# Performance work log

Measured on AMD Instinct MI355X. Metric: run time of the kernel, lower is better.

The kernel has to match this reference:

```python
import jax, jax.numpy as jnp
import numpy as np

EPS = 1e-5  # torch BatchNorm2d default eps
K = 16


def _bn_relu(x, gamma, beta):
    # training-mode BatchNorm over (B, N, k) per channel (last axis), biased variance
    mean = x.mean(axis=(0, 1, 2), keepdims=True)
    var = x.var(axis=(0, 1, 2), keepdims=True)
    xn = (x - mean) * jax.lax.rsqrt(var + EPS)
    return jax.nn.relu(xn * gamma + beta)


def _knn_idx(xyz, k):
    # squared pairwise distances (monotone in cdist p=2, same topk ordering)
    sq = jnp.sum(xyz * xyz, axis=-1)                       # (B, N)
    d2 = sq[:, :, None] + sq[:, None, :] - 2.0 * jnp.einsum('bnd,bmd->bnm', xyz, xyz)
    return jax.lax.top_k(-d2, k)[1]                        # (B, N, k) smallest dists


def setup_inputs() -> dict:
    key = jax.random.key(0)
    ks = jax.random.split(key, 4)
    B, N, C, O = 4, 4096, 64, 128
    return {
        'feats': jax.random.normal(ks[0], (B, N, C), jnp.float32),
        'xyz': jax.random.normal(ks[1], (B, N, 3), jnp.float32),
        'w1': jax.random.normal(ks[2], (O, 2 * C), jnp.float32) * 0.05,
        'gamma1': jnp.ones((O,), jnp.float32),
        'beta1': jnp.zeros((O,), jnp.float32),
        'w2': jax.random.normal(ks[3], (O, O), jnp.float32) * 0.05,
        'gamma2': jnp.ones((O,), jnp.float32),
        'beta2': jnp.zeros((O,), jnp.float32),
    }


def reference(feats, xyz, w1, gamma1, beta1, w2, gamma2, beta2):
    B, N, C = feats.shape
    k = min(K, N)
    idx = _knn_idx(xyz, k)                                  # (B, N, k)
    neighbor = jax.vmap(lambda f, i: f[i])(feats, idx)      # (B, N, k, C) gather
    center = feats[:, :, None, :]                           # (B, N, 1, C)
    edge = jnp.concatenate(
        [jnp.broadcast_to(center, neighbor.shape), neighbor - center], axis=-1
    )                                                       # (B, N, k, 2C)
    h = jnp.einsum('bnkc,oc->bnko', edge, w1)               # 1x1 conv #1
    h = _bn_relu(h, gamma1, beta1)
    h = jnp.einsum('bnkc,oc->bnko', h, w2)                  # 1x1 conv #2
    h = _bn_relu(h, gamma2, beta2)
    return h.max(axis=2)                                    # max over neighbors -> (B, N, O)
```

## Files before the change

### kernel.cpp

```cpp
#include <hip/hip_runtime.h>
#include <hip/hip_bf16.h>
#include <stdint.h>


#define B_ 4
#define N_ 4096
#define C_ 64
#define O_ 128
#define K_ 16
#define NQ_ (B_*N_)
#define ROWS_ (NQ_*K_)
#define EPS_ 1e-5f
#define M1_ 10
#define M2_ 20

typedef float f32x4 __attribute__((ext_vector_type(4)));
typedef short s16x8 __attribute__((ext_vector_type(8)));

__device__ __forceinline__ unsigned short f2bf(float f) {
  union { float f; uint32_t u; } x; x.f = f;
  uint32_t r = x.u + 0x7FFFu + ((x.u >> 16) & 1u);
  return (unsigned short)(r >> 16);
}
__device__ __forceinline__ uint32_t pack2(float a, float b) {
  return (uint32_t)f2bf(a) | ((uint32_t)f2bf(b) << 16);
}
__device__ __forceinline__ float bfl(uint32_t x) { return __uint_as_float(x << 16); }
__device__ __forceinline__ float bfh(uint32_t x) { return __uint_as_float(x & 0xFFFF0000u); }

template<bool SELF>
__device__ __forceinline__ void knn_scan(const float4* pts, int j0, int jq,
                                         float nx, float ny, float nz, float qw,
                                         float* lst) {
#pragma unroll 4
  for (int j = j0; j < j0 + N_/16; ++j) {
    float4 P = pts[j];
    float d2 = fmaf(P.z, nz, fmaf(P.y, ny, fmaf(P.x, nx, P.w + qw)));
    uint32_t kb = (__float_as_uint(d2) & 0xFFFFF000u) | (uint32_t)j;
    float k = __uint_as_float(kb);
    if (SELF) k = (j == jq) ? 1e30f : k;
#pragma unroll
    for (int s = M1_-1; s >= 1; --s)
      lst[s] = __builtin_amdgcn_fmed3f(lst[s-1], lst[s], k);
    lst[0] = fminf(lst[0], k);
  }
}

__global__ __launch_bounds__(1024) void knn_kernel(const float* __restrict__ xyz,
                                                   int* __restrict__ idx_out) {
  __shared__ float4 pts[N_];
  __shared__ float mbuf[8 * 64 * (M2_+1)];
  const int t = threadIdx.x;
  const int lane = t & 63;
  const int w = t >> 6;
  const int qbase = blockIdx.x * 64;
  const float* xb = xyz + (size_t)(qbase >> 12) * N_ * 3;
  for (int i = t; i < N_; i += 1024) {
    float x = xb[i*3+0], y = xb[i*3+1], z = xb[i*3+2];
    pts[i] = make_float4(x, y, z, fmaf(z, z, fmaf(y, y, x * x)));
  }
  __syncthreads();
  const int q0 = qbase & (N_-1);
  const int jq = q0 + lane;
  const float4 Q = pts[jq];
  float lst[M2_];
#pragma unroll
  for (int s = 0; s < M2_; ++s) lst[s] = 1e30f;
  const int j0 = w * (N_/16);
  if (w == (q0 >> 8)) knn_scan<true >(pts, j0, jq, -2.f*Q.x, -2.f*Q.y, -2.f*Q.z, Q.w, lst);
  else                knn_scan<false>(pts, j0, jq, -2.f*Q.x, -2.f*Q.y, -2.f*Q.z, Q.w, lst);
  for (int half = 8; half >= 1; half >>= 1) {
    const int cnt = (half == 8) ? M1_ : M2_;
    __syncthreads();
    if (w >= half && w < 2*half) {
      float* dst = mbuf + ((w - half) * 64 + lane) * (M2_+1);
      for (int s = 0; s < cnt; ++s) dst[s] = lst[s];
    }
    __syncthreads();
    if (w < half) {
      const float* src = mbuf + ((size_t)w * 64 + lane) * (M2_+1);
      for (int s = 0; s < cnt; ++s) {
        float k = src[s];
        if (!(k < lst[M2_-1])) break;
#pragma unroll
        for (int s2 = M2_-1; s2 >= 1; --s2)
          lst[s2] = __builtin_amdgcn_fmed3f(lst[s2-1], lst[s2], k);
        lst[0] = fminf(lst[0], k);
      }
    }
  }
  if (w == 0) {
    const double qx = (double)Q.x, qy = (double)Q.y, qz = (double)Q.z;
    double dk[M2_]; int jj[M2_]; int rk[M2_];
#pragma unroll
    for (int s = 0; s < M2_; ++s) {
      int j = (int)(__float_as_uint(lst[s]) & 0xFFFu);
      jj[s] = j;
      float4 P = pts[j];
      double dx = (double)P.x - qx, dy = (double)P.y - qy, dz = (double)P.z - qz;
      double d2 = fma(dz, dz, fma(dy, dy, dx * dx));
      dk[s] = __longlong_as_double(
          (__double_as_longlong(d2) & ~0xFFFLL) | (long long)j);
      rk[s] = 0;
    }
#pragma unroll
    for (int a = 0; a < M2_; ++a)
#pragma unroll
      for (int c = a + 1; c < M2_; ++c) {
        bool lt = dk[a] < dk[c];
        rk[c] += lt ? 1 : 0;
        rk[a] += lt ? 0 : 1;
      }
    int* op = idx_out + (size_t)(qbase + lane) * K_;
    op[0] = jq;
#pragma unroll
    for (int s = 0; s < M2_; ++s)
      if (rk[s] < K_-1) op[1 + rk[s]] = jj[s];
  }
}

__global__ __launch_bounds__(256) void uv_kernel(const float* __restrict__ feats,
                                                 const float* __restrict__ w1,
                                                 unsigned short* __restrict__ u,
                                                 unsigned short* __restrict__ v,
                                                 const float* __restrict__ w2,
                                                 unsigned short* __restrict__ w2bf,
                                                 float* __restrict__ stats1g,
                                                 float* __restrict__ stats2g) {
  const int t = threadIdx.x;
  if (blockIdx.x >= 256) {
    const int e = (blockIdx.x - 256) * 256 + t;
    w2bf[e] = f2bf(w2[e]);
    return;
  }
  __shared__ float wl[O_][129];
  __shared__ float fl[64][65];
  if (blockIdx.x == 0) { stats1g[t] = 0.f; stats2g[t] = 0.f; }
  for (int e = t; e < O_*128; e += 256) wl[e >> 7][e & 127] = w1[e];
  const int rbase = blockIdx.x * 64;
  for (int e = t; e < 64*C_; e += 256)
    fl[e >> 6][e & 63] = feats[(size_t)(rbase + (e >> 6)) * C_ + (e & 63)];
  __syncthreads();
  const int o = t & 127, rh = t >> 7;
  for (int r = rh; r < 64; r += 2) {
    float au = 0.f, av = 0.f;
#pragma unroll
    for (int c = 0; c < C_; ++c) {
      float f = fl[r][c];
      float wa = wl[o][c], wb = wl[o][C_ + c];
      au = fmaf(f, wa - wb, au);
      av = fmaf(f, wb, av);
    }
    size_t off = (size_t)(rbase + r) * O_ + o;
    u[off] = f2bf(au); v[off] = f2bf(av);
  }
}

__global__ __launch_bounds__(256) void stats1_kernel(const unsigned short* __restrict__ u,
                                                     const unsigned short* __restrict__ v,
                                                     const int* __restrict__ idx,
                                                     float* __restrict__ stats) {
  __shared__ float red[16][128][2];
  const int t = threadIdx.x;
  const int bid = blockIdx.x;
  const int blk = (bid & 7) * 64 + (bid >> 3);
  const int o8 = (t & 15) * 8, rg = t >> 4;
  const int rbase = blk * 32;
  float s[8], q[8];
#pragma unroll
  for (int i = 0; i < 8; ++i) { s[i] = 0.f; q[i] = 0.f; }
#pragma unroll
  for (int r = rg; r < 32; r += 16) {
    const int R = rbase + r;
    const int bb = R >> 12;
    uint4 uu = *(const uint4*)(u + (size_t)R * O_ + o8);
    float uf[8] = { bfl(uu.x), bfh(uu.x), bfl(uu.y), bfh(uu.y),
                    bfl(uu.z), bfh(uu.z), bfl(uu.w), bfh(uu.w) };
    int4 i0 = *(const int4*)(idx + (size_t)R * K_);
    int4 i1 = *(const int4*)(idx + (size_t)R * K_ + 4);
    int4 i2 = *(const int4*)(idx + (size_t)R * K_ + 8);
    int4 i3 = *(const int4*)(idx + (size_t)R * K_ + 12);
    int mi[16] = { i0.x,i0.y,i0.z,i0.w, i1.x,i1.y,i1.z,i1.w,
                   i2.x,i2.y,i2.z,i2.w, i3.x,i3.y,i3.z,i3.w };
    const unsigned short* vb = v + ((size_t)bb << 12) * O_ + o8;
#pragma unroll
    for (int k = 0; k < K_; ++k) {
      uint4 vv = *(const uint4*)(vb + (size_t)mi[k] * O_);
      float h;
      h = uf[0] + bfl(vv.x); s[0] += h; q[0] = fmaf(h, h, q[0]);
      h = uf[1] + bfh(vv.x); s[1] += h; q[1] = fmaf(h, h, q[1]);
      h = uf[2] + bfl(vv.y); s[2] += h; q[2] = fmaf(h, h, q[2]);
      h = uf[3] + bfh(vv.y); s[3] += h; q[3] = fmaf(h, h, q[3]);
      h = uf[4] + bfl(vv.z); s[4] += h; q[4] = fmaf(h, h, q[4]);
      h = uf[5] + bfh(vv.z); s[5] += h; q[5] = fmaf(h, h, q[5]);
      h = uf[6] + bfl(vv.w); s[6] += h; q[6] = fmaf(h, h, q[6]);
      h = uf[7] + bfh(vv.w); s[7] += h; q[7] = fmaf(h, h, q[7]);
    }
  }
#pragma unroll
  for (int i = 0; i < 8; ++i) { red[rg][o8 + i][0] = s[i]; red[rg][o8 + i][1] = q[i]; }
  __syncthreads();
  if (t < 128) {
    float ss = 0.f, qq = 0.f;
#pragma unroll
    for (int g = 0; g < 16; ++g) { ss += red[g][t][0]; qq += red[g][t][1]; }
    atomicAdd(&stats[t], ss);
    atomicAdd(&stats[O_ + t], qq);
  }
}

#define SWZ(row, byteoff) ((byteoff) ^ (((row) & 7) << 4))

__global__ __launch_bounds__(512, 2) void gemm2_kernel(
    const unsigned short* __restrict__ u, const unsigned short* __restrict__ v,
    const int* __restrict__ idx,
    const float* __restrict__ stats1g, const float* __restrict__ g1, const float* __restrict__ b1,
    const unsigned short* __restrict__ w2bf,
    float* __restrict__ stats2g, uint32_t* __restrict__ hmm) {
  __shared__ unsigned char Al[128 * 256];
  __shared__ unsigned char Bl[128 * 256];
  __shared__ unsigned short ul[1024];
  __shared__ float abl[256];
  __shared__ float cred[8][64][2];
  const int t = threadIdx.x;
  const int bid = blockIdx.x;
  const int blk = (bid & 7) * 64 + (bid >> 3);
  const float inv = 1.0f / (float)ROWS_;
  const int r = t >> 2, q = t & 3, ch = q * 32;
  const int rn = r >> 4, kk = r & 15;
  const int w = t >> 6, lane = t & 63;
  const int wm = w >> 1, wn = w & 1;
  const int r0 = lane & 15, kg = lane >> 4;

  int tile = blk * 4;
  int m_cur = idx[(size_t)(tile * 8 + rn) * K_ + kk];
  uint4 PV[4];
  {
    const int n0 = tile * 8 + rn;
    const unsigned short* vp = v + (((size_t)(n0 >> 12) << 12) + m_cur) * O_ + ch;
#pragma unroll
    for (int jj = 0; jj < 4; ++jj) PV[jj] = *(const uint4*)(vp + jj * 8);
  }
  uint4 pu1;
  if (t < 128) {
    pu1 = *(const uint4*)(u + (size_t)tile * 1024 + t * 8);
    float s = stats1g[t], s2 = stats1g[O_ + t];
    float mean = s * inv;
    float var = fmaf(-mean, mean, s2 * inv);
    float A = g1[t] * rsqrtf(var + EPS_);
    abl[t] = A;
    abl[O_ + t] = fmaf(-mean, A, b1[t]);
  }
  {
    const int o = t >> 2, c0 = q * 32;
    const unsigned short* src = w2bf + o * 128 + c0;
#pragma unroll
    for (int jj = 0; jj < 4; ++jj) {
      uint4 val = *(const uint4*)(src + jj * 8);
      *(uint4*)(Bl + SWZ(o, o * 256 + (c0 + jj * 8) * 2)) = val;
    }
  }
  if (t < 128) *(uint4*)(ul + t * 8) = pu1;
  int m_next = idx[(size_t)((tile + 1) * 8 + rn) * K_ + kk];

  float sacc[4] = {0.f,0.f,0.f,0.f}, sacc2[4] = {0.f,0.f,0.f,0.f};
#pragma unroll
  for (int ti = 0; ti < 4; ++ti) {
    __syncthreads();
    {
      const unsigned short* ulp = ul + rn * 128 + ch;
#pragma unroll
      for (int jj = 0; jj < 4; ++jj) {
        uint4 uu = *(const uint4*)(ulp + jj * 8);
        uint4 vv = PV[jj];
        const float* Ap = abl + ch + jj * 8;
        const float* Bp = abl + 128 + ch + jj * 8;
        float h0 = fmaxf(fmaf(bfl(uu.x) + bfl(vv.x), Ap[0], Bp[0]), 0.f);
        float h1 = fmaxf(fmaf(bfh(uu.x) + bfh(vv.x), Ap[1], Bp[1]), 0.f);
        float h2 = fmaxf(fmaf(bfl(uu.y) + bfl(vv.y), Ap[2], Bp[2]), 0.f);
        float h3 = fmaxf(fmaf(bfh(uu.y) + bfh(vv.y), Ap[3], Bp[3]), 0.f);
        float h4 = fmaxf(fmaf(bfl(uu.z) + bfl(vv.z), Ap[4], Bp[4]), 0.f);
        float h5 = fmaxf(fmaf(bfh(uu.z) + bfh(vv.z), Ap[5], Bp[5]), 0.f);
        float h6 = fmaxf(fmaf(bfl(uu.w) + bfl(vv.w), Ap[6], Bp[6]), 0.f);
        float h7 = fmaxf(fmaf(bfh(uu.w) + bfh(vv.w), Ap[7], Bp[7]), 0.f);
        *(uint4*)(Al + SWZ(r, r * 256 + (ch + jj * 8) * 2)) =
            make_uint4(pack2(h0,h1), pack2(h2,h3), pack2(h4,h5), pack2(h6,h7));
      }
    }
    __syncthreads();
    if (ti < 3) {
      const int nn = (tile + 1) * 8 + rn;
      const unsigned short* vp = v + (((size_t)(nn >> 12) << 12) + m_next) * O_ + ch;
#pragma unroll
      for (int jj = 0; jj < 4; ++jj) PV[jj] = *(const uint4*)(vp + jj * 8);
      if (t < 128) pu1 = *(const uint4*)(u + (size_t)(tile + 1) * 1024 + t * 8);
    }
    if (ti < 2) m_next = idx[(size_t)((tile + 2) * 8 + rn) * K_ + kk];
    f32x4 acc[2][4];
    f32x4 zero = {0.f, 0.f, 0.f, 0.f};
#pragma unroll
    for (int mi = 0; mi < 2; ++mi)
#pragma unroll
      for (int ni = 0; ni < 4; ++ni) acc[mi][ni] = zero;
#pragma unroll
    for (int ks = 0; ks < 4; ++ks) {
      const int cb = ks * 64 + kg * 16;
      s16x8 af[2], bf[4];
#pragma unroll
      for (int i = 0; i < 2; ++i) {
        const int ar = wm * 32 + i * 16 + r0;
        af[i] = *(const s16x8*)(Al + SWZ(ar, ar * 256 + cb));
      }
#pragma unroll
      for (int i = 0; i < 4; ++i) {
        const int br = wn * 64 + i * 16 + r0;
        bf[i] = *(const s16x8*)(Bl + SWZ(br, br * 256 + cb));
      }
#pragma unroll
      for (int mi = 0; mi < 2; ++mi)
#pragma unroll
        for (int ni = 0; ni < 4; ++ni)
          acc[mi][ni] = __builtin_amdgcn_mfma_f32_16x16x32_bf16(af[mi], bf[ni], acc[mi][ni], 0, 0, 0);
    }
    if (ti < 3 && t < 128) *(uint4*)(ul + t * 8) = pu1;
#pragma unroll
    for (int ni = 0; ni < 4; ++ni) {
      const int col = wn * 64 + ni * 16 + r0;
#pragma unroll
      for (int mi = 0; mi < 2; ++mi) {
        float a0 = acc[mi][ni][0], a1 = acc[mi][ni][1];
        float a2 = acc[mi][ni][2], a3 = acc[mi][ni][3];
        float mx = fmaxf(fmaxf(a0, a1), fmaxf(a2, a3));
        float mn = fminf(fminf(a0, a1), fminf(a2, a3));
        mx = fmaxf(mx, __shfl_xor(mx, 16));
        mx = fmaxf(mx, __shfl_xor(mx, 32));
        mn = fminf(mn, __shfl_xor(mn, 16));
        mn = fminf(mn, __shfl_xor(mn, 32));
        if (lane < 16)
          hmm[(size_t)(tile * 8 + wm * 2 + mi) * O_ + col] = pack2(mx, mn);
        sacc[ni] += (a0 + a1) + (a2 + a3);
        sacc2[ni] += fmaf(a0, a0, fmaf(a1, a1, fmaf(a2, a2, a3 * a3)));
      }
    }
    ++tile;
  }
#pragma unroll
  for (int ni = 0; ni < 4; ++ni) {
    float s = sacc[ni], s2 = sacc2[ni];
    s += __shfl_xor(s, 16);  s += __shfl_xor(s, 32);
    s2 += __shfl_xor(s2, 16); s2 += __shfl_xor(s2, 32);
    if (lane < 16) { cred[w][ni * 16 + r0][0] = s; cred[w][ni * 16 + r0][1] = s2; }
  }
  __syncthreads();
  if (t < 128) {
    const int o = t, wn0 = o >> 6, cl = o & 63;
    float s = 0.f, s2 = 0.f;
#pragma unroll
    for (int g = 0; g < 4; ++g) {
      s += cred[g * 2 + wn0][cl][0];
      s2 += cred[g * 2 + wn0][cl][1];
    }
    atomicAdd(&stats2g[o], s);
    atomicAdd(&stats2g[O_ + o], s2);
  }
}

__global__ __launch_bounds__(256) void finalize_kernel(const uint32_t* __restrict__ hmm,
        const float* __restrict__ stats2g, const float* __restrict__ g2,
        const float* __restrict__ b2, float* __restrict__ out) {
  __shared__ float Af[128], Bf[128];
  const int t = threadIdx.x;
  if (t < 128) {
    const float inv = 1.0f / (float)ROWS_;
    float s = stats2g[t], s2 = stats2g[O_ + t];
    float mean = s * inv;
    float var = fmaf(-mean, mean, s2 * inv);
    float A = g2[t] * rsqrtf(var + EPS_);
    Af[t] = A;
    Bf[t] = fmaf(-mean, A, b2[t]);
  }
  __syncthreads();
#pragma unroll
  for (int rep = 0; rep < 2; ++rep) {
    const int f4 = blockIdx.x * 512 + rep * 256 + t;
    uint4 p = ((const uint4*)hmm)[f4];
    const int c = (f4 & 31) * 4;
    float4 o4;
    { float A = Af[c+0], Bb = Bf[c+0]; float sel = (A >= 0.f) ? bfl(p.x) : bfh(p.x);
      o4.x = fmaxf(fmaf(A, sel, Bb), 0.f); }
    { float A = Af[c+1], Bb = Bf[c+1]; float sel = (A >= 0.f) ? bfl(p.y) : bfh(p.y);
      o4.y = fmaxf(fmaf(A, sel, Bb), 0.f); }
    { float A = Af[c+2], Bb = Bf[c+2]; float sel = (A >= 0.f) ? bfl(p.z) : bfh(p.z);
      o4.z = fmaxf(fmaf(A, sel, Bb), 0.f); }
    { float A = Af[c+3], Bb = Bf[c+3]; float sel = (A >= 0.f) ? bfl(p.w) : bfh(p.w);
      o4.w = fmaxf(fmaf(A, sel, Bb), 0.f); }
    ((float4*)out)[f4] = o4;
  }
}

extern "C" void kernel_launch(void* const* d_in, const int* in_sizes, int n_in,
                              void* d_out, int out_size, void* d_ws, size_t ws_size,
                              hipStream_t stream) {
  const float* feats = (const float*)d_in[0];
  const float* xyz   = (const float*)d_in[1];
  const float* w1    = (const float*)d_in[2];
  const float* g1    = (const float*)d_in[3];
  const float* b1    = (const float*)d_in[4];
  const float* w2    = (const float*)d_in[5];
  const float* g2    = (const float*)d_in[6];
  const float* b2    = (const float*)d_in[7];
  float* out = (float*)d_out;

  char* ws = (char*)d_ws;
  int*            idx     = (int*)(ws + 0);
  unsigned short* u       = (unsigned short*)(ws + (1ull << 20));
  unsigned short* v       = (unsigned short*)(ws + (5ull << 20));
  uint32_t*       hmm     = (uint32_t*)(ws + (9ull << 20));
  float*          stats1g = (float*)(ws + (17ull << 20));
  float*          stats2g = (float*)(ws + (17ull << 20) + 4096);
  unsigned short* w2bf    = (unsigned short*)(ws + (17ull << 20) + 8192);

  knn_kernel<<<256, 1024, 0, stream>>>(xyz, idx);
  uv_kernel<<<320, 256, 0, stream>>>(feats, w1, u, v, w2, w2bf, stats1g, stats2g);
  stats1_kernel<<<512, 256, 0, stream>>>(u, v, idx, stats1g);
  gemm2_kernel<<<512, 512, 0, stream>>>(u, v, idx, stats1g, g1, b1, w2bf, stats2g, hmm);
  finalize_kernel<<<1024, 256, 0, stream>>>(hmm, stats2g, g2, b2, out);
}
```

Baseline: 209.0 us.

## Compute u/v projection with bf16 MFMA and spread stats1 atomics over copies

The per-point u/v projection moves from a scalar fp32 FMA loop over padded LDS to bf16 MFMA 16x16x32 tiles. W1 differences and features are packed to bf16 into swizzled LDS, and the w2 conversion is folded into the first 64 blocks instead of extra blocks. stats1 now uses twice as many blocks with one row per thread group and writes into four partial-sum copies to reduce atomic contention, and gemm2 sums those copies. This lowers precision of the u/v inputs to the bf16 tensor path, though they were already stored as bf16.

```diff
diff --git a/kernel.cpp b/kernel.cpp
--- a/kernel.cpp
+++ b/kernel.cpp
@@ -27,6 +27,8 @@
 }
 __device__ __forceinline__ float bfl(uint32_t x) { return __uint_as_float(x << 16); }
 __device__ __forceinline__ float bfh(uint32_t x) { return __uint_as_float(x & 0xFFFF0000u); }
+
+#define SWZ(row, byteoff) ((byteoff) ^ (((row) & 7) << 4))
 
 template<bool SELF>
 __device__ __forceinline__ void knn_scan(const float4* pts, int j0, int jq,
@@ -127,32 +129,94 @@
                                                  unsigned short* __restrict__ w2bf,
                                                  float* __restrict__ stats1g,
                                                  float* __restrict__ stats2g) {
+  __shared__ unsigned char Wl[256 * 128];
+  __shared__ unsigned char Fl[64 * 128];
   const int t = threadIdx.x;
-  if (blockIdx.x >= 256) {
-    const int e = (blockIdx.x - 256) * 256 + t;
+  const int blk = blockIdx.x;
+  if (blk == 0) {
+    for (int e = t; e < 1024; e += 256) stats1g[e] = 0.f;
+    stats2g[t] = 0.f;
+  }
+  if (blk < 64) {
+    const int e = blk * 256 + t;
     w2bf[e] = f2bf(w2[e]);
-    return;
-  }
-  __shared__ float wl[O_][129];
-  __shared__ float fl[64][65];
-  if (blockIdx.x == 0) { stats1g[t] = 0.f; stats2g[t] = 0.f; }
-  for (int e = t; e < O_*128; e += 256) wl[e >> 7][e & 127] = w1[e];
-  const int rbase = blockIdx.x * 64;
-  for (int e = t; e < 64*C_; e += 256)
-    fl[e >> 6][e & 63] = feats[(size_t)(rbase + (e >> 6)) * C_ + (e & 63)];
+  }
+  {
+    const int ow = t;
+    if (ow < 128) {
+      const float* wa = w1 + ow * 128;
+      const float* wb = wa + 64;
+#pragma unroll
+      for (int g = 0; g < 8; ++g) {
+        float4 a0 = *(const float4*)(wa + g*8);
+        float4 a1 = *(const float4*)(wa + g*8 + 4);
+        float4 b0 = *(const float4*)(wb + g*8);
+        float4 b1 = *(const float4*)(wb + g*8 + 4);
+        *(uint4*)(Wl + SWZ(ow, ow*128 + g*16)) =
+            make_uint4(pack2(a0.x-b0.x, a0.y-b0.y), pack2(a0.z-b0.z, a0.w-b0.w),
+                       pack2(a1.x-b1.x, a1.y-b1.y), pack2(a1.z-b1.z, a1.w-b1.w));
+      }
+    } else {
+      const float* wb = w1 + (ow - 128) * 128 + 64;
+#pragma unroll
+      for (int g = 0; g < 8; ++g) {
+        float4 a0 = *(const float4*)(wb + g*8);
+        float4 a1 = *(const float4*)(wb + g*8 + 4);
+        *(uint4*)(Wl + SWZ(ow, ow*128 + g*16)) =
+            make_uint4(pack2(a0.x, a0.y), pack2(a0.z, a0.w),
+                       pack2(a1.x, a1.y), pack2(a1.z, a1.w));
+      }
+    }
+  }
+  {
+    const int row = t >> 2, q = t & 3;
+    const float* fp = feats + (size_t)(blk * 64 + row) * 64 + q * 16;
+#pragma unroll
+    for (int g = 0; g < 2; ++g) {
+      float4 a = *(const float4*)(fp + g*8);
+      float4 b = *(const float4*)(fp + g*8 + 4);
+      *(uint4*)(Fl + SWZ(row, row*128 + q*32 + g*16)) =
+          make_uint4(pack2(a.x,a.y), pack2(a.z,a.w), pack2(b.x,b.y), pack2(b.z,b.w));
+    }
+  }
   __syncthreads();
-  const int o = t & 127, rh = t >> 7;
-  for (int r = rh; r < 64; r += 2) {
-    float au = 0.f, av = 0.f;
-#pragma unroll
-    for (int c = 0; c < C_; ++c) {
-      float f = fl[r][c];
-      float wa = wl[o][c], wb = wl[o][C_ + c];
-      au = fmaf(f, wa - wb, au);
-      av = fmaf(f, wb, av);
-    }
-    size_t off = (size_t)(rbase + r) * O_ + o;
-    u[off] = f2bf(au); v[off] = f2bf(av);
+  const int w = t >> 6, lane = t & 63;
+  const int r0 = lane & 15, kg = lane >> 4;
+  f32x4 acc[4][4];
+  f32x4 zero = {0.f, 0.f, 0.f, 0.f};
+#pragma unroll
+  for (int mi = 0; mi < 4; ++mi)
+#pragma unroll
+    for (int ni = 0; ni < 4; ++ni) acc[mi][ni] = zero;
+#pragma unroll
+  for (int ks = 0; ks < 2; ++ks) {
+    const int cb = ks * 64 + kg * 16;
+    s16x8 af[4], bf[4];
+#pragma unroll
+    for (int i = 0; i < 4; ++i) {
+      const int ar = i * 16 + r0;
+      af[i] = *(const s16x8*)(Fl + SWZ(ar, ar*128 + cb));
+      const int br = w * 64 + i * 16 + r0;
+      bf[i] = *(const s16x8*)(Wl + SWZ(br, br*128 + cb));
+    }
+#pragma unroll
+    for (int mi = 0; mi < 4; ++mi)
+#pragma unroll
+      for (int ni = 0; ni < 4; ++ni)
+        acc[mi][ni] = __builtin_amdgcn_mfma_f32_16x16x32_bf16(af[mi], bf[ni], acc[mi][ni], 0, 0, 0);
+  }
+  const int rbase = blk * 64;
+#pragma unroll
+  for (int ni = 0; ni < 4; ++ni) {
+    const int col = w * 64 + ni * 16 + r0;
+    unsigned short* dst = (col < 128) ? (u + col) : (v + col - 128);
+#pragma unroll
+    for (int mi = 0; mi < 4; ++mi)
+#pragma unroll
+      for (int i = 0; i < 4; ++i) {
+        const int row = rbase + mi * 16 + kg * 4 + i;
+        dst[(size_t)row * O_] = f2bf(acc[mi][ni][i]);
+      }
   }
 }
 
@@ -163,39 +227,35 @@
   __shared__ float red[16][128][2];
   const int t = threadIdx.x;
   const int bid = blockIdx.x;
-  const int blk = (bid & 7) * 64 + (bid >> 3);
+  const int blk = (bid & 7) * 128 + (bid >> 3);
   const int o8 = (t & 15) * 8, rg = t >> 4;
-  const int rbase = blk * 32;
+  const int R = blk * 16 + rg;
+  const int bb = R >> 12;
   float s[8], q[8];
 #pragma unroll
   for (int i = 0; i < 8; ++i) { s[i] = 0.f; q[i] = 0.f; }
-#pragma unroll
-  for (int r = rg; r < 32; r += 16) {
-    const int R = rbase + r;
-    const int bb = R >> 12;
-    uint4 uu = *(const uint4*)(u + (size_t)R * O_ + o8);
-    float uf[8] = { bfl(uu.x), bfh(uu.x), bfl(uu.y), bfh(uu.y),
-                    bfl(uu.z), bfh(uu.z), bfl(uu.w), bfh(uu.w) };
-    int4 i0 = *(const int4*)(idx + (size_t)R * K_);
-    int4 i1 = *(const int4*)(idx + (size_t)R * K_ + 4);
-    int4 i2 = *(const int4*)(idx + (size_t)R * K_ + 8);
-    int4 i3 = *(const int4*)(idx + (size_t)R * K_ + 12);
-    int mi[16] = { i0.x,i0.y,i0.z,i0.w, i1.x,i1.y,i1.z,i1.w,
-                   i2.x,i2.y,i2.z,i2.w, i3.x,i3.y,i3.z,i3.w };
-    const unsigned short* vb = v + ((size_t)bb << 12) * O_ + o8;
-#pragma unroll
-    for (int k = 0; k < K_; ++k) {
-      uint4 vv = *(const uint4*)(vb + (size_t)mi[k] * O_);
-      float h;
-      h = uf[0] + bfl(vv.x); s[0] += h; q[0] = fmaf(h, h, q[0]);
-      h = uf[1] + bfh(vv.x); s[1] += h; q[1] = fmaf(h, h, q[1]);
-      h = uf[2] + bfl(vv.y); s[2] += h; q[2] = fmaf(h, h, q[2]);
-      h = uf[3] + bfh(vv.y); s[3] += h; q[3] = fmaf(h, h, q[3]);
-      h = uf[4] + bfl(vv.z); s[4] += h; q[4] = fmaf(h, h, q[4]);
-      h = uf[5] + bfh(vv.z); s[5] += h; q[5] = fmaf(h, h, q[5]);
-      h = uf[6] + bfl(vv.w); s[6] += h; q[6] = fmaf(h, h, q[6]);
-      h = uf[7] + bfh(vv.w); s[7] += h; q[7] = fmaf(h, h, q[7]);
-    }
+  uint4 uu = *(const uint4*)(u + (size_t)R * O_ + o8);
+  float uf[8] = { bfl(uu.x), bfh(uu.x), bfl(uu.y), bfh(uu.y),
+                  bfl(uu.z), bfh(uu.z), bfl(uu.w), bfh(uu.w) };
+  int4 i0 = *(const int4*)(idx + (size_t)R * K_);
+  int4 i1 = *(const int4*)(idx + (size_t)R * K_ + 4);
+  int4 i2 = *(const int4*)(idx + (size_t)R * K_ + 8);
+  int4 i3 = *(const int4*)(idx + (size_t)R * K_ + 12);
+  int mi[16] = { i0.x,i0.y,i0.z,i0.w, i1.x,i1.y,i1.z,i1.w,
+                 i2.x,i2.y,i2.z,i2.w, i3.x,i3.y,i3.z,i3.w };
+  const unsigned short* vb = v + ((size_t)bb << 12) * O_ + o8;
+#pragma unroll
+  for (int k = 0; k < K_; ++k) {
+    uint4 vv = *(const uint4*)(vb + (size_t)mi[k] * O_);
+    float h;
+    h = uf[0] + bfl(vv.x); s[0] += h; q[0] = fmaf(h, h, q[0]);
+    h = uf[1] + bfh(vv.x); s[1] += h; q[1] = fmaf(h, h, q[1]);
+    h = uf[2] + bfl(vv.y); s[2] += h; q[2] = fmaf(h, h, q[2]);
+    h = uf[3] + bfh(vv.y); s[3] += h; q[3] = fmaf(h, h, q[3]);
+    h = uf[4] + bfl(vv.z); s[4] += h; q[4] = fmaf(h, h, q[4]);
+    h = uf[5] + bfh(vv.z); s[5] += h; q[5] = fmaf(h, h, q[5]);
+    h = uf[6] + bfl(vv.w); s[6] += h; q[6] = fmaf(h, h, q[6]);
+    h = uf[7] + bfh(vv.w); s[7] += h; q[7] = fmaf(h, h, q[7]);
   }
 #pragma unroll
   for (int i = 0; i < 8; ++i) { red[rg][o8 + i][0] = s[i]; red[rg][o8 + i][1] = q[i]; }
@@ -204,12 +264,11 @@
     float ss = 0.f, qq = 0.f;
 #pragma unroll
     for (int g = 0; g < 16; ++g) { ss += red[g][t][0]; qq += red[g][t][1]; }
-    atomicAdd(&stats[t], ss);
-    atomicAdd(&stats[O_ + t], qq);
-  }
-}
-
-#define SWZ(row, byteoff) ((byteoff) ^ (((row) & 7) << 4))
+    float* sc = stats + (bid & 3) * 256;
+    atomicAdd(&sc[t], ss);
+    atomicAdd(&sc[128 + t], qq);
+  }
+}
 
 __global__ __launch_bounds__(512, 2) void gemm2_kernel(
     const unsigned short* __restrict__ u, const unsigned short* __restrict__ v,
@@ -244,7 +303,12 @@
   uint4 pu1;
   if (t < 128) {
     pu1 = *(const uint4*)(u + (size_t)tile * 1024 + t * 8);
-    float s = stats1g[t], s2 = stats1g[O_ + t];
+    float s = 0.f, s2 = 0.f;
+#pragma unroll
+    for (int c = 0; c < 4; ++c) {
+      s += stats1g[c * 256 + t];
+      s2 += stats1g[c * 256 + 128 + t];
+    }
     float mean = s * inv;
     float var = fmaf(-mean, mean, s2 * inv);
     float A = g1[t] * rsqrtf(var + EPS_);
@@ -421,8 +485,8 @@
   unsigned short* w2bf    = (unsigned short*)(ws + (17ull << 20) + 8192);
 
   knn_kernel<<<256, 1024, 0, stream>>>(xyz, idx);
-  uv_kernel<<<320, 256, 0, stream>>>(feats, w1, u, v, w2, w2bf, stats1g, stats2g);
-  stats1_kernel<<<512, 256, 0, stream>>>(u, v, idx, stats1g);
+  uv_kernel<<<256, 256, 0, stream>>>(feats, w1, u, v, w2, w2bf, stats1g, stats2g);
+  stats1_kernel<<<1024, 256, 0, stream>>>(u, v, idx, stats1g);
   gemm2_kernel<<<512, 512, 0, stream>>>(u, v, idx, stats1g, g1, b1, w2bf, stats2g, hmm);
   finalize_kernel<<<1024, 256, 0, stream>>>(hmm, stats2g, g2, b2, out);
 }
```

Result: faster. 175.3 us (-16.1%).
